# Performance work log

Measured on AMD Instinct MI355X. Metric: run time of the kernel, lower is better.

Reference implementation:

```python
import jax, jax.numpy as jnp
import numpy as np

D_MODEL = 1024
N_HEADS = 16
D_HEAD = D_MODEL // N_HEADS
D_FF = 4096
MAX_ITERS = 2
B, T = 8, 1024
LN_EPS = 1e-5


def _layernorm(x, g, b):
    m = jnp.mean(x, axis=-1, keepdims=True)
    v = jnp.mean(jnp.square(x - m), axis=-1, keepdims=True)
    return (x - m) * jax.lax.rsqrt(v + LN_EPS) * g + b


def setup_inputs() -> dict:
    key = jax.random.key(0)
    ks = jax.random.split(key, 16)
    s = 0.02
    inp = {
        "z": jax.random.normal(ks[0], (B, T, D_MODEL), dtype=jnp.float32),
        # per-head Q/K/V projections stacked over heads: [H, D, Dh], bias [H, Dh]
        "Wq": jax.random.normal(ks[1], (N_HEADS, D_MODEL, D_HEAD), dtype=jnp.float32) * s,
        "bq": jnp.zeros((N_HEADS, D_HEAD), dtype=jnp.float32),
        "Wk": jax.random.normal(ks[2], (N_HEADS, D_MODEL, D_HEAD), dtype=jnp.float32) * s,
        "bk": jnp.zeros((N_HEADS, D_HEAD), dtype=jnp.float32),
        "Wv": jax.random.normal(ks[3], (N_HEADS, D_MODEL, D_HEAD), dtype=jnp.float32) * s,
        "bv": jnp.zeros((N_HEADS, D_HEAD), dtype=jnp.float32),
        "Wo": jax.random.normal(ks[4], (D_MODEL, D_MODEL), dtype=jnp.float32) * s,
        "bo": jnp.zeros((D_MODEL,), dtype=jnp.float32),
        "W1": jax.random.normal(ks[5], (D_MODEL, D_FF), dtype=jnp.float32) * s,
        "b1": jnp.zeros((D_FF,), dtype=jnp.float32),
        "W2": jax.random.normal(ks[6], (D_FF, D_MODEL), dtype=jnp.float32) * s,
        "b2": jnp.zeros((D_MODEL,), dtype=jnp.float32),
        "g1": jnp.ones((D_MODEL,), dtype=jnp.float32),
        "be1": jnp.zeros((D_MODEL,), dtype=jnp.float32),
        "g2": jnp.ones((D_MODEL,), dtype=jnp.float32),
        "be2": jnp.zeros((D_MODEL,), dtype=jnp.float32),
    }
    return inp


def reference(z, Wq, bq, Wk, bk, Wv, bv, Wo, bo, W1, b1, W2, b2, g1, be1, g2, be2):
    # Controller outputs (alphas/state/aux) are unused by the original forward -> omitted.
    # Dropout is inference-identity.
    scale = 1.0 / jnp.sqrt(jnp.asarray(D_HEAD, dtype=z.dtype))
    z_refined = z
    for _ in range(MAX_ITERS):
        # batched per-head projections: [B,H,T,Dh]
        q = jnp.einsum('btd,hdk->bhtk', z, Wq) + bq[None, :, None, :]
        k = jnp.einsum('btd,hdk->bhtk', z, Wk) + bk[None, :, None, :]
        v = jnp.einsum('btd,hdk->bhtk', z, Wv) + bv[None, :, None, :]
        scores = jnp.einsum('bhtk,bhsk->bhts', q, k) * scale  # [B,H,T,T]
        attn = jax.nn.softmax(scores, axis=-1)
        o = jnp.einsum('bhts,bhsk->bhtk', attn, v)  # [B,H,T,Dh]
        # concat heads in order (matches torch.cat over head list)
        o = jnp.transpose(o, (0, 2, 1, 3)).reshape(z.shape[0], z.shape[1], D_MODEL)
        attn_out = o @ Wo + bo
        z = _layernorm(z + attn_out, g1, be1)
        z_refined = z
        ffn = jnp.maximum(z @ W1 + b1, 0.0) @ W2 + b2
        z = _layernorm(z + ffn, g2, be2)
    return z_refined
```

## Files before the change

### kernel.cpp

```cpp
#include <hip/hip_runtime.h>
#include <hip/hip_bf16.h>

typedef __bf16 bf16t;
typedef bf16t bf16x4 __attribute__((ext_vector_type(4)));
typedef bf16t bf16x8 __attribute__((ext_vector_type(8)));
typedef float f32x4 __attribute__((ext_vector_type(4)));

#define BT 8192
#define TT 1024
#define DM 1024
#define DFF 4096
#define QSCALE 0.18033688011112042f

static __device__ __forceinline__ f32x4 mfma16(bf16x8 a, bf16x8 b, f32x4 c) {
  return __builtin_amdgcn_mfma_f32_16x16x32_bf16(a, b, c, 0, 0, 0);
}
static __device__ __forceinline__ f32x4 f4zero() {
  f32x4 z = {0.f, 0.f, 0.f, 0.f};
  return z;
}
static __device__ __forceinline__ f32x4 vmax4(f32x4 a, f32x4 b) {
  f32x4 r;
#pragma unroll
  for (int i = 0; i < 4; i++) r[i] = fmaxf(a[i], b[i]);
  return r;
}
static __device__ __forceinline__ void gld16(const bf16t* g, bf16t* l) {
  __builtin_amdgcn_global_load_lds((const __attribute__((address_space(1))) void*)g,
                                   (__attribute__((address_space(3))) void*)l, 16, 0, 0);
}
static __device__ __forceinline__ int cperm(int c) {
  return (c & ~31) + (((c >> 2) & 3) << 3) + (((c >> 4) & 1) << 2) + (c & 3);
}

__global__ __launch_bounds__(256) void cvtz_kernel(const float* __restrict__ in,
                                                   bf16t* __restrict__ outp,
                                                   bf16t* __restrict__ outn, long n) {
  long i = ((long)blockIdx.x * 256 + threadIdx.x) * 4;
  if (i >= n) return;
  f32x4 v = *(const f32x4*)&in[i];
  bf16x4 o = {(bf16t)v[0], (bf16t)v[1], (bf16t)v[2], (bf16t)v[3]};
  *(bf16x4*)&outn[i] = o;
  int lo = (int)(i & 1023);
  long p = (i - lo) + cperm(lo);
  *(bf16x4*)&outp[p] = o;
}

__global__ __launch_bounds__(256) void tcvt_kernel(const float* __restrict__ in,
                                                   bf16t* __restrict__ out, int M, int N) {
  __shared__ float T[64][65];
  const int t = threadIdx.x;
  const int ty = t >> 6, tx = t & 63;
  const long n0 = (long)blockIdx.x * 64, m0 = (long)blockIdx.y * 64;
#pragma unroll
  for (int p = 0; p < 16; ++p) {
    int a = ty * 16 + p;
    T[a][tx] = in[(m0 + a) * N + n0 + tx];
  }
  __syncthreads();
#pragma unroll
  for (int p = 0; p < 16; ++p) {
    int r = ty * 16 + p;
    out[(n0 + r) * M + m0 + cperm(tx)] = (bf16t)T[tx][r];
  }
}

__global__ __launch_bounds__(256) void pack_qkv_t_kernel(const float* __restrict__ Wq,
                                                         const float* __restrict__ Wk,
                                                         const float* __restrict__ Wv,
                                                         bf16t* __restrict__ WT) {
  __shared__ float T[64][65];
  const int bx = blockIdx.x;
  const int sel = bx >> 4, h = bx & 15;
  const float* src = ((sel == 0) ? Wq : (sel == 1) ? Wk : Wv) + (long)h * 65536;
  const long nbase = (long)sel * 1024 + h * 64;
  const long m0 = (long)blockIdx.y * 64;
  const int t = threadIdx.x;
  const int ty = t >> 6, tx = t & 63;
#pragma unroll
  for (int p = 0; p < 16; ++p) {
    int a = ty * 16 + p;
    T[a][tx] = src[(m0 + a) * 64 + tx];
  }
  __syncthreads();
#pragma unroll
  for (int p = 0; p < 16; ++p) {
    int r = ty * 16 + p;
    WT[(nbase + r) * 1024 + m0 + cperm(tx)] = (bf16t)T[tx][r];
  }
}

__global__ __launch_bounds__(256) void pack_bias_kernel(const float* __restrict__ bq,
                                                        const float* __restrict__ bk,
                                                        const float* __restrict__ bv,
                                                        float* __restrict__ bqkv) {
  int i = blockIdx.x * 256 + threadIdx.x;
  if (i >= 3072) return;
  int sel = i >> 10, c = i & 1023;
  bqkv[i] = ((sel == 0) ? bq : (sel == 1) ? bk : bv)[c];
}

template <int EPI>
__global__ __launch_bounds__(256, 2) void gemmBig_kernel(
    const bf16t* __restrict__ A, const bf16t* __restrict__ Bt,
    const float* __restrict__ bias, bf16t* __restrict__ Cout,
    bf16t* __restrict__ vTout, int M, int N, int K) {
  __shared__ __align__(16) bf16t As[2 * 256 * 32];
  __shared__ __align__(16) bf16t Bs[2 * 128 * 32];
  const int tid = threadIdx.x;
  const int lane = tid & 63;
  const int wid = tid >> 6;
  const int wm = wid >> 1;
  const int wn = wid & 1;
  const int g = lane >> 4, lr = lane & 15;

  const int gy = M >> 8;
  const int nwg = gridDim.x;
  const int chunk = nwg >> 3;
  const int wg = blockIdx.x;
  const int lid = (wg & 7) * chunk + (wg >> 3);
  const int gsz = gy << 3;
  const int group = lid / gsz;
  const int rem = lid - group * gsz;
  const int rr = rem >> 3;
  const int cc = (group << 3) + (rem & 7);
  const long brow = (long)rr * 256;
  const long bcol = (long)cc * 128;

  f32x4 acc[8][4];
#pragma unroll
  for (int i = 0; i < 8; i++)
#pragma unroll
    for (int j = 0; j < 4; j++) acc[i][j] = f4zero();

  const int srow = tid >> 2;
  const int csrc = (tid & 3) ^ ((tid >> 3) & 3);
  const bf16t* gA = &A[(brow + srow) * (long)K + 8 * csrc];
  const bf16t* gB = &Bt[(bcol + srow) * (long)K + 8 * csrc];
  bf16t* lA = As + wid * 512;
  bf16t* lB = Bs + wid * 512;

  auto stage = [&](int buf, int k0) {
#pragma unroll
    for (int c = 0; c < 4; ++c)
      gld16(gA + k0 + (long)(c * 64) * K, lA + buf * 8192 + c * 2048);
#pragma unroll
    for (int c = 0; c < 2; ++c)
      gld16(gB + k0 + (long)(c * 64) * K, lB + buf * 4096 + c * 2048);
  };
  auto ldfA = [&](int buf, int row) -> bf16x8 {
    return *(const bf16x8*)(As + buf * 8192 + row * 32 + ((((row >> 1) ^ g) & 3) << 3));
  };
  auto ldfB = [&](int buf, int row) -> bf16x8 {
    return *(const bf16x8*)(Bs + buf * 4096 + row * 32 + ((((row >> 1) ^ g) & 3) << 3));
  };

  const int nt = K >> 5;
  stage(0, 0);
  __syncthreads();

  for (int t = 0; t < nt; ++t) {
    const int buf = t & 1;
    if (t + 1 < nt) stage(buf ^ 1, (t + 1) << 5);

    bf16x8 a[8], b[4];
#pragma unroll
    for (int i = 0; i < 8; i++) a[i] = ldfA(buf, wm * 128 + i * 16 + lr);
#pragma unroll
    for (int j = 0; j < 4; j++) b[j] = ldfB(buf, wn * 64 + j * 16 + lr);
#pragma unroll
    for (int i = 0; i < 8; i++)
#pragma unroll
      for (int j = 0; j < 4; j++) acc[i][j] = mfma16(a[i], b[j], acc[i][j]);

    __syncthreads();
  }

#pragma unroll
  for (int j = 0; j < 4; j++) {
    int col = (int)bcol + wn * 64 + j * 16 + lr;
    float bval = bias ? bias[col] : 0.f;
#pragma unroll
    for (int i = 0; i < 8; i++) {
      long row0 = brow + wm * 128 + i * 16 + 4 * g;
      if (EPI == 0 && col >= 2048) {
        int h2 = (col - 2048) >> 6, d = col & 63;
        long bb = row0 >> 10;
        int t0 = (int)(row0 & 1023);
        long idx = ((((bb << 4) + h2) << 6) + d) * 1024 + cperm(t0);
        bf16x4 ov;
#pragma unroll
        for (int r2 = 0; r2 < 4; r2++) ov[r2] = (bf16t)(acc[i][j][r2] + bval);
        *(bf16x4*)&vTout[idx] = ov;
      } else {
#pragma unroll
        for (int r2 = 0; r2 < 4; r2++) {
          long row = row0 + r2;
          float v = acc[i][j][r2] + bval;
          if (EPI == 0) {
            float vv = (col < 1024) ? v * QSCALE : v;
            Cout[row * N + cperm(col)] = (bf16t)vv;
          } else {
            Cout[row * N + cperm(col)] = (bf16t)fmaxf(v, 0.f);
          }
        }
      }
    }
  }
}

template <int EPI>
__global__ __launch_bounds__(256) void gemm_kernel(
    const bf16t* __restrict__ A, const bf16t* __restrict__ Bt,
    const float* __restrict__ bias, const bf16t* __restrict__ resid,
    void* __restrict__ Cout, int M, int N, int K) {
  __shared__ __align__(16) bf16t As[3 * 128 * 32];
  __shared__ __align__(16) bf16t Bs[3 * 128 * 32];
  const int tid = threadIdx.x;
  const int lane = tid & 63;
  const int wid = tid >> 6;
  const int wr = wid >> 1, wc = wid & 1;
  const int g = lane >> 4, lr = lane & 15;

  const int gy = M >> 7;
  const int nwg = gridDim.x;
  const int chunk = nwg >> 3;
  const int wg = blockIdx.x;
  const int lid = (wg & 7) * chunk + (wg >> 3);
  const int gsz = gy << 3;
  const int group = lid / gsz;
  const int rem = lid - group * gsz;
  const int rr = rem >> 3;
  const int cc = (group << 3) + (rem & 7);
  const long brow = (long)rr * 128;
  const long bcol = (long)cc * 128;

  f32x4 acc[4][4];
#pragma unroll
  for (int i = 0; i < 4; i++)
#pragma unroll
    for (int j = 0; j < 4; j++) acc[i][j] = f4zero();

  const int srow = tid >> 2;
  const int csrc = (tid & 3) ^ ((tid >> 3) & 3);
  const bf16t* gA = &A[(brow + srow) * (long)K + 8 * csrc];
  const bf16t* gB = &Bt[(bcol + srow) * (long)K + 8 * csrc];
  bf16t* lA = As + wid * 512;
  bf16t* lB = Bs + wid * 512;

  auto stage = [&](int buf, int k0) {
    gld16(gA + k0, lA + buf * 4096);
    gld16(gA + k0 + (long)64 * K, lA + buf * 4096 + 2048);
    gld16(gB + k0, lB + buf * 4096);
    gld16(gB + k0 + (long)64 * K, lB + buf * 4096 + 2048);
  };
  auto ldf = [&](const bf16t* buf, int row) -> bf16x8 {
    return *(const bf16x8*)(buf + row * 32 + ((((row >> 1) ^ g) & 3) << 3));
  };

  const int nt = K >> 5;
  stage(0, 0);
  stage(1, 32);
  asm volatile("s_waitcnt vmcnt(4)" ::: "memory");
  __builtin_amdgcn_s_barrier();
  __builtin_amdgcn_sched_barrier(0);

  for (int t = 0; t < nt; ++t) {
    const int k2 = (t + 2) << 5;
    const bool pf = (k2 < K);
    if (pf) stage((t + 2) % 3, k2);

    const bf16t* bufA = As + (t % 3) * 4096;
    const bf16t* bufB = Bs + (t % 3) * 4096;
    bf16x8 af[4], bfv[4];
#pragma unroll
    for (int i = 0; i < 4; i++) af[i] = ldf(bufA, wr * 64 + i * 16 + lr);
#pragma unroll
    for (int j = 0; j < 4; j++) bfv[j] = ldf(bufB, wc * 64 + j * 16 + lr);
#pragma unroll
    for (int i = 0; i < 4; i++)
#pragma unroll
      for (int j = 0; j < 4; j++) acc[i][j] = mfma16(af[i], bfv[j], acc[i][j]);

    if (t + 1 < nt) {
      if (pf)
        asm volatile("s_waitcnt vmcnt(4)" ::: "memory");
      else
        asm volatile("s_waitcnt vmcnt(0)" ::: "memory");
      __builtin_amdgcn_s_barrier();
      __builtin_amdgcn_sched_barrier(0);
    }
  }

#pragma unroll
  for (int j = 0; j < 4; j++) {
    int col = (int)bcol + wc * 64 + j * 16 + lr;
    float bval = bias ? bias[col] : 0.f;
#pragma unroll
    for (int i = 0; i < 4; i++) {
      long row0 = brow + wr * 64 + i * 16 + 4 * g;
#pragma unroll
      for (int r2 = 0; r2 < 4; r2++) {
        long row = row0 + r2;
        float v = acc[i][j][r2] + bval;
        ((bf16t*)Cout)[row * N + col] = (bf16t)(v + (float)resid[row * N + col]);
      }
    }
  }
}

__global__ __launch_bounds__(256) void attn_kernel(const bf16t* __restrict__ qkv,
                                                   const bf16t* __restrict__ vT,
                                                   bf16t* __restrict__ o) {
  const int bh = blockIdx.x;
  const int b = bh >> 4, h = bh & 15;
  const int qt = blockIdx.y;
  const int tid = threadIdx.x;
  const int lane = tid & 63;
  const int w = tid >> 6;
  const int g = lane >> 4, lr = lane & 15;

  __shared__ __align__(16) bf16t Qs[2 * 64 * 32];
  __shared__ __align__(16) bf16t Ks[2][2 * 64 * 32];
  __shared__ __align__(16) bf16t Vs[2][2 * 64 * 32];

  const long rowbase = (long)b * TT;
  const long qrow0 = rowbase + (long)qt * 64;

  const int sq = tid >> 2;
  const int sco = (((tid & 3) ^ ((tid >> 3) & 3))) * 8;

  const bf16t* qsrc = &qkv[(qrow0 + sq) * 3072 + h * 64 + sco];
  const bf16t* ksrc = &qkv[(rowbase + sq) * 3072 + 1024 + h * 64 + sco];
  const bf16t* vsrc = &vT[((long)bh * 64 + sq) * 1024 + sco];
  const int wbase = w * 512;

  auto stageQ = [&]() {
    gld16(qsrc, Qs + wbase);
    gld16(qsrc + 32, Qs + 2048 + wbase);
  };
  auto stageK = [&](int buf, int kt) {
    const bf16t* s = ksrc + (long)kt * 64 * 3072;
    gld16(s, Ks[buf] + wbase);
    gld16(s + 32, Ks[buf] + 2048 + wbase);
  };
  auto stageV = [&](int buf, int kt) {
    const bf16t* s = vsrc + kt * 64;
    gld16(s, Vs[buf] + wbase);
    gld16(s + 32, Vs[buf] + 2048 + wbase);
  };
  auto ldf = [&](const bf16t* base, int hh, int row) -> bf16x8 {
    return *(const bf16x8*)(base + hh * 2048 + row * 32 + ((((row >> 1) ^ g) & 3) << 3));
  };

  stageQ();
  stageK(0, 0);
  stageV(0, 0);
  __syncthreads();

  const int qr = w * 16 + lr;
  const bf16x8 qb_lo = ldf(Qs, 0, qr);
  const bf16x8 qb_hi = ldf(Qs, 1, qr);

  f32x4 acc_o[4];
#pragma unroll
  for (int j = 0; j < 4; j++) acc_o[j] = f4zero();
  float mrun = -1e30f, lrun = 0.f;

  int cur = 0;
  for (int kt = 0; kt < 16; ++kt) {
    if (kt < 15) {
      stageK(cur ^ 1, kt + 1);
      stageV(cur ^ 1, kt + 1);
    }

    f32x4 s[4];
#pragma unroll
    for (int jt = 0; jt < 4; jt++) {
      int krow = jt * 16 + lr;
      bf16x8 ka_lo = ldf(Ks[cur], 0, krow);
      bf16x8 ka_hi = ldf(Ks[cur], 1, krow);
      f32x4 t = f4zero();
      t = mfma16(ka_lo, qb_lo, t);
      t = mfma16(ka_hi, qb_hi, t);
      s[jt] = t;
    }

    f32x4 mv = vmax4(vmax4(s[0], s[1]), vmax4(s[2], s[3]));
    float tm = fmaxf(fmaxf(mv[0], mv[1]), fmaxf(mv[2], mv[3]));
    tm = fmaxf(tm, __shfl_xor(tm, 16, 64));
    tm = fmaxf(tm, __shfl_xor(tm, 32, 64));

    if (__any(tm > mrun + 11.5f)) {
      float mnew = fmaxf(mrun, tm);
      float corr = __builtin_amdgcn_exp2f(mrun - mnew);
      mrun = mnew;
      lrun *= corr;
#pragma unroll
      for (int r = 0; r < 4; r++) {
        float cq = __shfl(corr, 20 * g + r, 64);
#pragma unroll
        for (int dt = 0; dt < 4; dt++) acc_o[dt][r] *= cq;
      }
    }

    f32x4 sv = f4zero();
#pragma unroll
    for (int jt = 0; jt < 4; jt++)
#pragma unroll
      for (int r = 0; r < 4; r++) {
        float pv = __builtin_amdgcn_exp2f(s[jt][r] - mrun);
        s[jt][r] = pv;
        sv[r] += pv;
      }
    float tsum = sv[0] + sv[1] + sv[2] + sv[3];
    tsum += __shfl_xor(tsum, 16, 64);
    tsum += __shfl_xor(tsum, 32, 64);
    lrun += tsum;

    bf16x8 pa0, pa1;
#pragma unroll
    for (int r = 0; r < 4; r++) {
      pa0[r] = (bf16t)s[0][r];
      pa0[r + 4] = (bf16t)s[1][r];
      pa1[r] = (bf16t)s[2][r];
      pa1[r + 4] = (bf16t)s[3][r];
    }

#pragma unroll
    for (int dt = 0; dt < 4; dt++) {
      int vrow = dt * 16 + lr;
      bf16x8 vb_lo = ldf(Vs[cur], 0, vrow);
      bf16x8 vb_hi = ldf(Vs[cur], 1, vrow);
      acc_o[dt] = mfma16(pa0, vb_lo, acc_o[dt]);
      acc_o[dt] = mfma16(pa1, vb_hi, acc_o[dt]);
    }

    __syncthreads();
    cur ^= 1;
  }

  float inv = 1.0f / lrun;
#pragma unroll
  for (int r = 0; r < 4; r++) {
    float iq = __shfl(inv, 20 * g + r, 64);
    long row = qrow0 + w * 16 + 4 * g + r;
#pragma unroll
    for (int dt = 0; dt < 4; dt++) {
      o[row * (long)DM + cperm(h * 64 + dt * 16 + lr)] = (bf16t)(acc_o[dt][r] * iq);
    }
  }
}

__global__ __launch_bounds__(256) void ln_kernel(const bf16t* __restrict__ x,
                                                 const float* __restrict__ gamma,
                                                 const float* __restrict__ beta,
                                                 bf16t* __restrict__ out_act,
                                                 bf16t* __restrict__ out_res,
                                                 float* __restrict__ out_f32) {
  const long row = blockIdx.x;
  const int tid = threadIdx.x;
  const int idx = tid * 4;
  bf16x4 xv = *(const bf16x4*)&x[row * DM + idx];
  float v[4];
#pragma unroll
  for (int c = 0; c < 4; c++) v[c] = (float)xv[c];
  float s = v[0] + v[1] + v[2] + v[3];
  float ss = v[0] * v[0] + v[1] * v[1] + v[2] * v[2] + v[3] * v[3];
#pragma unroll
  for (int m = 1; m < 64; m <<= 1) {
    s += __shfl_xor(s, m, 64);
    ss += __shfl_xor(ss, m, 64);
  }
  __shared__ float red[8];
  const int w = tid >> 6, lane = tid & 63;
  if (lane == 0) {
    red[w] = s;
    red[4 + w] = ss;
  }
  __syncthreads();
  s = red[0] + red[1] + red[2] + red[3];
  ss = red[4] + red[5] + red[6] + red[7];
  float mean = s * (1.f / DM);
  float var = ss * (1.f / DM) - mean * mean;
  float inv = rsqrtf(var + 1e-5f);
  f32x4 ga = *(const f32x4*)&gamma[idx];
  f32x4 be = *(const f32x4*)&beta[idx];
  float y[4];
#pragma unroll
  for (int c = 0; c < 4; c++) y[c] = (v[c] - mean) * inv * ga[c] + be[c];
  if (out_act) {
    bf16x4 ob = {(bf16t)y[0], (bf16t)y[1], (bf16t)y[2], (bf16t)y[3]};
    *(bf16x4*)&out_act[row * DM + cperm(idx)] = ob;
  }
  if (out_res) {
    bf16x4 ob = {(bf16t)y[0], (bf16t)y[1], (bf16t)y[2], (bf16t)y[3]};
    *(bf16x4*)&out_res[row * DM + idx] = ob;
  }
  if (out_f32) {
    f32x4 of = {y[0], y[1], y[2], y[3]};
    *(f32x4*)&out_f32[row * DM + idx] = of;
  }
}

extern "C" void kernel_launch(void* const* d_in, const int* in_sizes, int n_in,
                              void* d_out, int out_size, void* d_ws, size_t ws_size,
                              hipStream_t stream) {
  const float* z = (const float*)d_in[0];
  const float* Wq = (const float*)d_in[1];
  const float* bq = (const float*)d_in[2];
  const float* Wk = (const float*)d_in[3];
  const float* bk = (const float*)d_in[4];
  const float* Wv = (const float*)d_in[5];
  const float* bv = (const float*)d_in[6];
  const float* Wo = (const float*)d_in[7];
  const float* bo = (const float*)d_in[8];
  const float* W1 = (const float*)d_in[9];
  const float* b1 = (const float*)d_in[10];
  const float* W2 = (const float*)d_in[11];
  const float* b2 = (const float*)d_in[12];
  const float* g1 = (const float*)d_in[13];
  const float* be1 = (const float*)d_in[14];
  const float* g2 = (const float*)d_in[15];
  const float* be2 = (const float*)d_in[16];

  char* p = (char*)d_ws;
  auto alloc = [&](size_t bytes) {
    char* r = p;
    p += (bytes + 255) & ~(size_t)255;
    return r;
  };
  bf16t* wqkvT = (bf16t*)alloc((size_t)3072 * 1024 * 2);
  float* bqkv = (float*)alloc((size_t)3072 * 4);
  bf16t* woT = (bf16t*)alloc((size_t)1024 * 1024 * 2);
  bf16t* w1T = (bf16t*)alloc((size_t)4096 * 1024 * 2);
  bf16t* w2T = (bf16t*)alloc((size_t)1024 * 4096 * 2);
  bf16t* act = (bf16t*)alloc((size_t)BT * 1024 * 2);
  bf16t* zbf = (bf16t*)alloc((size_t)BT * 1024 * 2);
  bf16t* obuf = (bf16t*)alloc((size_t)BT * 1024 * 2);
  bf16t* big = (bf16t*)alloc((size_t)BT * 4096 * 2);
  bf16t* tbuf = (bf16t*)alloc((size_t)BT * 1024 * 2);
  bf16t* residf = (bf16t*)alloc((size_t)BT * 1024 * 2);
  bf16t* vT = (bf16t*)tbuf;

  pack_qkv_t_kernel<<<dim3(48, 16), dim3(256), 0, stream>>>(Wq, Wk, Wv, wqkvT);
  pack_bias_kernel<<<dim3(12), dim3(256), 0, stream>>>(bq, bk, bv, bqkv);
  tcvt_kernel<<<dim3(16, 16), dim3(256), 0, stream>>>(Wo, woT, 1024, 1024);
  tcvt_kernel<<<dim3(64, 16), dim3(256), 0, stream>>>(W1, w1T, 1024, 4096);
  tcvt_kernel<<<dim3(16, 64), dim3(256), 0, stream>>>(W2, w2T, 4096, 1024);
  cvtz_kernel<<<dim3(8192), dim3(256), 0, stream>>>(z, act, zbf, (long)BT * 1024);

  for (int iter = 0; iter < 2; ++iter) {
    gemmBig_kernel<0><<<dim3(768), dim3(256), 0, stream>>>(
        act, wqkvT, bqkv, big, vT, BT, 3072, 1024);
    attn_kernel<<<dim3(128, 16), dim3(256), 0, stream>>>(big, vT, obuf);
    const bf16t* rsrc = (iter == 0) ? zbf : residf;
    gemm_kernel<2><<<dim3(512), dim3(256), 0, stream>>>(
        obuf, woT, bo, rsrc, (void*)tbuf, BT, 1024, 1024);
    if (iter == 1) {
      ln_kernel<<<dim3(8192), dim3(256), 0, stream>>>(tbuf, g1, be1, (bf16t*)nullptr,
                                                      (bf16t*)nullptr, (float*)d_out);
      break;
    }
    ln_kernel<<<dim3(8192), dim3(256), 0, stream>>>(tbuf, g1, be1, act, residf,
                                                    (float*)nullptr);
    gemmBig_kernel<1><<<dim3(1024), dim3(256), 0, stream>>>(
        act, w1T, b1, big, (bf16t*)nullptr, BT, 4096, 1024);
    gemm_kernel<2><<<dim3(512), dim3(256), 0, stream>>>(
        big, w2T, b2, residf, (void*)tbuf, BT, 1024, 4096);
    ln_kernel<<<dim3(8192), dim3(256), 0, stream>>>(tbuf, g2, be2, act, residf,
                                                    (float*)nullptr);
  }
}
```

Before: 583.6 us.

## Replace QKV/FFN1 GEMM with 256x256-tile 8-wave ping-pong pipelined kernel

```diff
diff --git a/kernel.cpp b/kernel.cpp
--- a/kernel.cpp
+++ b/kernel.cpp
@@ -101,17 +101,17 @@
 }
 
 template <int EPI>
-__global__ __launch_bounds__(256, 2) void gemmBig_kernel(
+__global__ __launch_bounds__(512, 2) void gemm8p_kernel(
     const bf16t* __restrict__ A, const bf16t* __restrict__ Bt,
     const float* __restrict__ bias, bf16t* __restrict__ Cout,
     bf16t* __restrict__ vTout, int M, int N, int K) {
-  __shared__ __align__(16) bf16t As[2 * 256 * 32];
-  __shared__ __align__(16) bf16t Bs[2 * 128 * 32];
+  __shared__ __align__(16) bf16t As[2][2][256 * 32];
+  __shared__ __align__(16) bf16t Bs[2][2][256 * 32];
   const int tid = threadIdx.x;
   const int lane = tid & 63;
   const int wid = tid >> 6;
-  const int wm = wid >> 1;
-  const int wn = wid & 1;
+  const int wm = wid >> 2;
+  const int wn = wid & 3;
   const int g = lane >> 4, lr = lane & 15;
 
   const int gy = M >> 8;
@@ -119,13 +119,13 @@
   const int chunk = nwg >> 3;
   const int wg = blockIdx.x;
   const int lid = (wg & 7) * chunk + (wg >> 3);
-  const int gsz = gy << 3;
+  const int gsz = gy << 2;
   const int group = lid / gsz;
   const int rem = lid - group * gsz;
-  const int rr = rem >> 3;
-  const int cc = (group << 3) + (rem & 7);
+  const int rr = rem >> 2;
+  const int cc = (group << 2) + (rem & 3);
   const long brow = (long)rr * 256;
-  const long bcol = (long)cc * 128;
+  const long bcol = (long)cc * 256;
 
   f32x4 acc[8][4];
 #pragma unroll
@@ -137,43 +137,143 @@
   const int csrc = (tid & 3) ^ ((tid >> 3) & 3);
   const bf16t* gA = &A[(brow + srow) * (long)K + 8 * csrc];
   const bf16t* gB = &Bt[(bcol + srow) * (long)K + 8 * csrc];
-  bf16t* lA = As + wid * 512;
-  bf16t* lB = Bs + wid * 512;
-
-  auto stage = [&](int buf, int k0) {
-#pragma unroll
-    for (int c = 0; c < 4; ++c)
-      gld16(gA + k0 + (long)(c * 64) * K, lA + buf * 8192 + c * 2048);
-#pragma unroll
-    for (int c = 0; c < 2; ++c)
-      gld16(gB + k0 + (long)(c * 64) * K, lB + buf * 4096 + c * 2048);
-  };
-  auto ldfA = [&](int buf, int row) -> bf16x8 {
-    return *(const bf16x8*)(As + buf * 8192 + row * 32 + ((((row >> 1) ^ g) & 3) << 3));
-  };
-  auto ldfB = [&](int buf, int row) -> bf16x8 {
-    return *(const bf16x8*)(Bs + buf * 4096 + row * 32 + ((((row >> 1) ^ g) & 3) << 3));
-  };
-
-  const int nt = K >> 5;
-  stage(0, 0);
-  __syncthreads();
-
-  for (int t = 0; t < nt; ++t) {
-    const int buf = t & 1;
-    if (t + 1 < nt) stage(buf ^ 1, (t + 1) << 5);
-
-    bf16x8 a[8], b[4];
-#pragma unroll
-    for (int i = 0; i < 8; i++) a[i] = ldfA(buf, wm * 128 + i * 16 + lr);
-#pragma unroll
-    for (int j = 0; j < 4; j++) b[j] = ldfB(buf, wn * 64 + j * 16 + lr);
-#pragma unroll
-    for (int i = 0; i < 8; i++)
-#pragma unroll
-      for (int j = 0; j < 4; j++) acc[i][j] = mfma16(a[i], b[j], acc[i][j]);
-
-    __syncthreads();
+
+  auto stageA = [&](int b, int h, int k0) {
+    bf16t* dst = &As[b][h][wid * 512];
+    const bf16t* src = gA + k0 + 32 * h;
+    gld16(src, dst);
+    gld16(src + (long)128 * K, dst + 4096);
+  };
+  auto stageB = [&](int b, int h, int k0) {
+    bf16t* dst = &Bs[b][h][wid * 512];
+    const bf16t* src = gB + k0 + 32 * h;
+    gld16(src, dst);
+    gld16(src + (long)128 * K, dst + 4096);
+  };
+  auto lda = [&](int b, int s, int row) -> bf16x8 {
+    return *(const bf16x8*)(&As[b][s][row * 32 + ((((row >> 1) ^ g) & 3) << 3)]);
+  };
+  auto ldb = [&](int b, int s, int row) -> bf16x8 {
+    return *(const bf16x8*)(&Bs[b][s][row * 32 + ((((row >> 1) ^ g) & 3) << 3)]);
+  };
+
+  const int nt = K >> 6;
+  stageA(0, 0, 0);
+  stageB(0, 0, 0);
+  stageA(0, 1, 0);
+  stageB(0, 1, 0);
+  asm volatile("s_waitcnt vmcnt(4)" ::: "memory");
+  __builtin_amdgcn_s_barrier();
+  __builtin_amdgcn_sched_barrier(0);
+
+  for (int kt = 0; kt < nt; ++kt) {
+    const int buf = kt & 1;
+    const int nb = buf ^ 1;
+    const int nk0 = (kt + 1) << 6;
+    const bool pf = (kt + 1 < nt);
+    bf16x8 b0, b1, b2, b3;
+
+    {
+      b0 = ldb(buf, 0, wn * 64 + 0 * 16 + lr);
+      b1 = ldb(buf, 0, wn * 64 + 1 * 16 + lr);
+      b2 = ldb(buf, 0, wn * 64 + 2 * 16 + lr);
+      b3 = ldb(buf, 0, wn * 64 + 3 * 16 + lr);
+      bf16x8 a0 = lda(buf, 0, wm * 128 + 0 * 16 + lr);
+      bf16x8 a1 = lda(buf, 0, wm * 128 + 1 * 16 + lr);
+      bf16x8 a2 = lda(buf, 0, wm * 128 + 2 * 16 + lr);
+      bf16x8 a3 = lda(buf, 0, wm * 128 + 3 * 16 + lr);
+      if (pf) stageA(nb, 0, nk0);
+      __builtin_amdgcn_s_barrier();
+      asm volatile("s_waitcnt lgkmcnt(0)" ::: "memory");
+      __builtin_amdgcn_sched_barrier(0);
+      __builtin_amdgcn_s_setprio(1);
+      acc[0][0] = mfma16(a0, b0, acc[0][0]); acc[0][1] = mfma16(a0, b1, acc[0][1]);
+      acc[0][2] = mfma16(a0, b2, acc[0][2]); acc[0][3] = mfma16(a0, b3, acc[0][3]);
+      acc[1][0] = mfma16(a1, b0, acc[1][0]); acc[1][1] = mfma16(a1, b1, acc[1][1]);
+      acc[1][2] = mfma16(a1, b2, acc[1][2]); acc[1][3] = mfma16(a1, b3, acc[1][3]);
+      acc[2][0] = mfma16(a2, b0, acc[2][0]); acc[2][1] = mfma16(a2, b1, acc[2][1]);
+      acc[2][2] = mfma16(a2, b2, acc[2][2]); acc[2][3] = mfma16(a2, b3, acc[2][3]);
+      acc[3][0] = mfma16(a3, b0, acc[3][0]); acc[3][1] = mfma16(a3, b1, acc[3][1]);
+      acc[3][2] = mfma16(a3, b2, acc[3][2]); acc[3][3] = mfma16(a3, b3, acc[3][3]);
+      __builtin_amdgcn_s_setprio(0);
+      __builtin_amdgcn_s_barrier();
+    }
+    {
+      bf16x8 a4 = lda(buf, 0, wm * 128 + 4 * 16 + lr);
+      bf16x8 a5 = lda(buf, 0, wm * 128 + 5 * 16 + lr);
+      bf16x8 a6 = lda(buf, 0, wm * 128 + 6 * 16 + lr);
+      bf16x8 a7 = lda(buf, 0, wm * 128 + 7 * 16 + lr);
+      if (pf) stageB(nb, 0, nk0);
+      __builtin_amdgcn_s_barrier();
+      asm volatile("s_waitcnt lgkmcnt(0)" ::: "memory");
+      __builtin_amdgcn_sched_barrier(0);
+      __builtin_amdgcn_s_setprio(1);
+      acc[4][0] = mfma16(a4, b0, acc[4][0]); acc[4][1] = mfma16(a4, b1, acc[4][1]);
+      acc[4][2] = mfma16(a4, b2, acc[4][2]); acc[4][3] = mfma16(a4, b3, acc[4][3]);
+      acc[5][0] = mfma16(a5, b0, acc[5][0]); acc[5][1] = mfma16(a5, b1, acc[5][1]);
+      acc[5][2] = mfma16(a5, b2, acc[5][2]); acc[5][3] = mfma16(a5, b3, acc[5][3]);
+      acc[6][0] = mfma16(a6, b0, acc[6][0]); acc[6][1] = mfma16(a6, b1, acc[6][1]);
+      acc[6][2] = mfma16(a6, b2, acc[6][2]); acc[6][3] = mfma16(a6, b3, acc[6][3]);
+      acc[7][0] = mfma16(a7, b0, acc[7][0]); acc[7][1] = mfma16(a7, b1, acc[7][1]);
+      acc[7][2] = mfma16(a7, b2, acc[7][2]); acc[7][3] = mfma16(a7, b3, acc[7][3]);
+      __builtin_amdgcn_s_setprio(0);
+      if (pf)
+        asm volatile("s_waitcnt vmcnt(4)" ::: "memory");
+      else
+        asm volatile("s_waitcnt vmcnt(0)" ::: "memory");
+      __builtin_amdgcn_s_barrier();
+      __builtin_amdgcn_sched_barrier(0);
+    }
+    {
+      b0 = ldb(buf, 1, wn * 64 + 0 * 16 + lr);
+      b1 = ldb(buf, 1, wn * 64 + 1 * 16 + lr);
+      b2 = ldb(buf, 1, wn * 64 + 2 * 16 + lr);
+      b3 = ldb(buf, 1, wn * 64 + 3 * 16 + lr);
+      bf16x8 a0 = lda(buf, 1, wm * 128 + 0 * 16 + lr);
+      bf16x8 a1 = lda(buf, 1, wm * 128 + 1 * 16 + lr);
+      bf16x8 a2 = lda(buf, 1, wm * 128 + 2 * 16 + lr);
+      bf16x8 a3 = lda(buf, 1, wm * 128 + 3 * 16 + lr);
+      if (pf) stageA(nb, 1, nk0);
+      __builtin_amdgcn_s_barrier();
+      asm volatile("s_waitcnt lgkmcnt(0)" ::: "memory");
+      __builtin_amdgcn_sched_barrier(0);
+      __builtin_amdgcn_s_setprio(1);
+      acc[0][0] = mfma16(a0, b0, acc[0][0]); acc[0][1] = mfma16(a0, b1, acc[0][1]);
+      acc[0][2] = mfma16(a0, b2, acc[0][2]); acc[0][3] = mfma16(a0, b3, acc[0][3]);
+      acc[1][0] = mfma16(a1, b0, acc[1][0]); acc[1][1] = mfma16(a1, b1, acc[1][1]);
+      acc[1][2] = mfma16(a1, b2, acc[1][2]); acc[1][3] = mfma16(a1, b3, acc[1][3]);
+      acc[2][0] = mfma16(a2, b0, acc[2][0]); acc[2][1] = mfma16(a2, b1, acc[2][1]);
+      acc[2][2] = mfma16(a2, b2, acc[2][2]); acc[2][3] = mfma16(a2, b3, acc[2][3]);
+      acc[3][0] = mfma16(a3, b0, acc[3][0]); acc[3][1] = mfma16(a3, b1, acc[3][1]);
+      acc[3][2] = mfma16(a3, b2, acc[3][2]); acc[3][3] = mfma16(a3, b3, acc[3][3]);
+      __builtin_amdgcn_s_setprio(0);
+      __builtin_amdgcn_s_barrier();
+    }
+    {
+      bf16x8 a4 = lda(buf, 1, wm * 128 + 4 * 16 + lr);
+      bf16x8 a5 = lda(buf, 1, wm * 128 + 5 * 16 + lr);
+      bf16x8 a6 = lda(buf, 1, wm * 128 + 6 * 16 + lr);
+      bf16x8 a7 = lda(buf, 1, wm * 128 + 7 * 16 + lr);
+      if (pf) stageB(nb, 1, nk0);
+      __builtin_amdgcn_s_barrier();
+      asm volatile("s_waitcnt lgkmcnt(0)" ::: "memory");
+      __builtin_amdgcn_sched_barrier(0);
+      __builtin_amdgcn_s_setprio(1);
+      acc[4][0] = mfma16(a4, b0, acc[4][0]); acc[4][1] = mfma16(a4, b1, acc[4][1]);
+      acc[4][2] = mfma16(a4, b2, acc[4][2]); acc[4][3] = mfma16(a4, b3, acc[4][3]);
+      acc[5][0] = mfma16(a5, b0, acc[5][0]); acc[5][1] = mfma16(a5, b1, acc[5][1]);
+      acc[5][2] = mfma16(a5, b2, acc[5][2]); acc[5][3] = mfma16(a5, b3, acc[5][3]);
+      acc[6][0] = mfma16(a6, b0, acc[6][0]); acc[6][1] = mfma16(a6, b1, acc[6][1]);
+      acc[6][2] = mfma16(a6, b2, acc[6][2]); acc[6][3] = mfma16(a6, b3, acc[6][3]);
+      acc[7][0] = mfma16(a7, b0, acc[7][0]); acc[7][1] = mfma16(a7, b1, acc[7][1]);
+      acc[7][2] = mfma16(a7, b2, acc[7][2]); acc[7][3] = mfma16(a7, b3, acc[7][3]);
+      __builtin_amdgcn_s_setprio(0);
+      if (pf) {
+        asm volatile("s_waitcnt vmcnt(4)" ::: "memory");
+        __builtin_amdgcn_s_barrier();
+        __builtin_amdgcn_sched_barrier(0);
+      }
+    }
   }
 
 #pragma unroll
@@ -209,11 +309,10 @@
   }
 }
 
-template <int EPI>
 __global__ __launch_bounds__(256) void gemm_kernel(
     const bf16t* __restrict__ A, const bf16t* __restrict__ Bt,
     const float* __restrict__ bias, const bf16t* __restrict__ resid,
-    void* __restrict__ Cout, int M, int N, int K) {
+    bf16t* __restrict__ Cout, int M, int N, int K) {
   __shared__ __align__(16) bf16t As[3 * 128 * 32];
   __shared__ __align__(16) bf16t Bs[3 * 128 * 32];
   const int tid = threadIdx.x;
@@ -303,7 +402,7 @@
       for (int r2 = 0; r2 < 4; r2++) {
         long row = row0 + r2;
         float v = acc[i][j][r2] + bval;
-        ((bf16t*)Cout)[row * N + col] = (bf16t)(v + (float)resid[row * N + col]);
+        Cout[row * N + col] = (bf16t)(v + (float)resid[row * N + col]);
       }
     }
   }
@@ -551,12 +650,12 @@
   cvtz_kernel<<<dim3(8192), dim3(256), 0, stream>>>(z, act, zbf, (long)BT * 1024);
 
   for (int iter = 0; iter < 2; ++iter) {
-    gemmBig_kernel<0><<<dim3(768), dim3(256), 0, stream>>>(
+    gemm8p_kernel<0><<<dim3(384), dim3(512), 0, stream>>>(
         act, wqkvT, bqkv, big, vT, BT, 3072, 1024);
     attn_kernel<<<dim3(128, 16), dim3(256), 0, stream>>>(big, vT, obuf);
     const bf16t* rsrc = (iter == 0) ? zbf : residf;
-    gemm_kernel<2><<<dim3(512), dim3(256), 0, stream>>>(
-        obuf, woT, bo, rsrc, (void*)tbuf, BT, 1024, 1024);
+    gemm_kernel<<<dim3(512), dim3(256), 0, stream>>>(
+        obuf, woT, bo, rsrc, tbuf, BT, 1024, 1024);
     if (iter == 1) {
       ln_kernel<<<dim3(8192), dim3(256), 0, stream>>>(tbuf, g1, be1, (bf16t*)nullptr,
                                                       (bf16t*)nullptr, (float*)d_out);
@@ -564,10 +663,10 @@
     }
     ln_kernel<<<dim3(8192), dim3(256), 0, stream>>>(tbuf, g1, be1, act, residf,
                                                     (float*)nullptr);
-    gemmBig_kernel<1><<<dim3(1024), dim3(256), 0, stream>>>(
+    gemm8p_kernel<1><<<dim3(512), dim3(512), 0, stream>>>(
         act, w1T, b1, big, (bf16t*)nullptr, BT, 4096, 1024);
-    gemm_kernel<2><<<dim3(512), dim3(256), 0, stream>>>(
-        big, w2T, b2, residf, (void*)tbuf, BT, 1024, 4096);
+    gemm_kernel<<<dim3(512), dim3(256), 0, stream>>>(
+        big, w2T, b2, residf, tbuf, BT, 1024, 4096);
     ln_kernel<<<dim3(8192), dim3(256), 0, stream>>>(tbuf, g2, be2, act, residf,
                                                     (float*)nullptr);
   }
```

After: 584.8 us. Within noise of the previous version (+0.2%).
